# Kernel optimization log

Measured on AMD Instinct MI355X. Metric: run time of the kernel, lower is better.

The kernel has to match this reference:

```python
import jax, jax.numpy as jnp
import numpy as np

N_NODE, N_NET, E = 100000, 20000, 200000
H_NODE, H_NET, H_PIN = 64, 32, 16
O_NODE, O_NET = 32, 64


def setup_inputs() -> dict:
    key = jax.random.key(0)
    ks = jax.random.split(key, 8)
    return {
        'node_feat': jax.random.normal(ks[0], (N_NODE, H_NODE), jnp.float32),
        'net_feat': jax.random.normal(ks[1], (N_NET, H_NET), jnp.float32),
        'pin_feat': jax.random.normal(ks[2], (E, H_PIN), jnp.float32),
        'edge_node': jax.random.randint(ks[3], (E,), 0, N_NODE, jnp.int32),
        'edge_net': jax.random.randint(ks[4], (E,), 0, N_NET, jnp.int32),
        'W1': jax.random.normal(ks[5], (H_NODE, O_NET), jnp.float32) * 0.05,
        'b1': jnp.zeros((O_NET,), jnp.float32),
        'W2': jax.random.normal(ks[6], (H_PIN, H_NET * O_NODE), jnp.float32) * 0.05,
        'b2': jnp.zeros((H_NET * O_NODE,), jnp.float32),
        'b_nn': jnp.zeros((O_NODE,), jnp.float32),
    }


def reference(node_feat, net_feat, pin_feat, edge_node, edge_net, W1, b1, W2, b2, b_nn):
    ones = jnp.ones((E,), node_feat.dtype)
    # ---- relation 'pins': node -> net, DGL GraphConv with norm='both' ----
    out_deg = jnp.clip(jax.ops.segment_sum(ones, edge_node, num_segments=N_NODE), 1.0)  # src out-degree
    in_deg = jnp.clip(jax.ops.segment_sum(ones, edge_net, num_segments=N_NET), 1.0)     # dst in-degree
    src = node_feat * jax.lax.rsqrt(out_deg)[:, None]                                   # [N_node, H_node]
    agg = jax.ops.segment_sum(src[edge_node], edge_net, num_segments=N_NET)             # [N_net, H_node]
    net_out = (agg * jax.lax.rsqrt(in_deg)[:, None]) @ W1 + b1                           # [N_net, O_net]
    # ---- relation 'pinned': net -> node, DGL NNConv (mean aggregator) ----
    We = (pin_feat @ W2 + b2).reshape(E, H_NET, O_NODE)                                  # per-edge weight matrix
    msg = jnp.einsum('ei,eio->eo', net_feat[edge_net], We)                               # [E, O_node]
    node_deg = jnp.clip(jax.ops.segment_sum(ones, edge_node, num_segments=N_NODE), 1.0)
    node_out = jax.ops.segment_sum(msg, edge_node, num_segments=N_NODE) / node_deg[:, None] + b_nn
    return node_out, net_out
```

## Files before the change

kernel.cpp:

```cpp
#include <hip/hip_runtime.h>
#include <hip/hip_bf16.h>

#define N_NODE 100000
#define N_NET  20000
#define NE     200000
#define H_NODE 64
#define H_NET  32
#define H_PIN  16
#define O_NODE 32
#define O_NET  64
#define CSR_STRIDE 64


#define OFF_NETCNT  6400000
#define OFF_CSR     7680000
#define OFF_Z       17920000
#define OFF_C       38400000
#define OFF_XB      40960000
#define ZERO_BYTES  7680000

static __device__ __forceinline__ unsigned short f2bf(float f) {
    unsigned int u = __float_as_uint(f);
    u += 0x7fff + ((u >> 16) & 1);
    return (unsigned short)(u >> 16);
}
static __device__ __forceinline__ float bf2f(unsigned short h) {
    return __uint_as_float(((unsigned int)h) << 16);
}

#define EDGE_BLKS 782

__global__ void k_edge(const int* __restrict__ en, const int* __restrict__ em,
                       int* __restrict__ node_deg, int* __restrict__ net_cnt,
                       int2* __restrict__ csr) {
    int e = blockIdx.x * 256 + threadIdx.x;
    if (e < NE) {
        int v = en[e], n = em[e];
        atomicAdd(&node_deg[v << 4], 1);
        int slot = atomicAdd(&net_cnt[n << 4], 1);
        if (slot < CSR_STRIDE) csr[n * CSR_STRIDE + slot] = make_int2(e, v);
    }
}

#define DNS_Z_BLKS    1250
#define DNS_INIT_BLKS 3125
#define DNS_XB_BLKS   1563
#define ZNPB 16

__global__ void k_dense(const float* __restrict__ net_feat,
                        const float* __restrict__ node_feat,
                        const float* __restrict__ W2, const float* __restrict__ b2,
                        unsigned short* __restrict__ Zb, float* __restrict__ C,
                        unsigned short* __restrict__ Xb,
                        const float* __restrict__ b_nn,
                        float* __restrict__ out_node) {
    int t = threadIdx.x, b = blockIdx.x;
    if (b < DNS_Z_BLKS) {
        __shared__ float sy[ZNPB][H_NET];
        int base = b * ZNPB;
        for (int idx = t; idx < ZNPB * H_NET; idx += 256)
            sy[idx >> 5][idx & 31] = net_feat[(base + (idx >> 5)) * H_NET + (idx & 31)];
        __syncthreads();
        int o = t & 31, k4 = (t >> 5) & 3, rep = t >> 7;
        const float* w2p = W2 + (k4 * 4) * 1024 + o;
        float4 acc[8];
#pragma unroll
        for (int g = 0; g < 8; g++) acc[g] = make_float4(0.f, 0.f, 0.f, 0.f);
#pragma unroll 4
        for (int i = 0; i < H_NET; i++) {
            float w0 = w2p[0 * 1024 + i * 32];
            float w1 = w2p[1 * 1024 + i * 32];
            float w2v = w2p[2 * 1024 + i * 32];
            float w3 = w2p[3 * 1024 + i * 32];
#pragma unroll
            for (int g = 0; g < 8; g++) {
                float y = sy[rep * 8 + g][i];
                acc[g].x += w0 * y; acc[g].y += w1 * y;
                acc[g].z += w2v * y; acc[g].w += w3 * y;
            }
        }
#pragma unroll
        for (int g = 0; g < 8; g++) {
            int n = base + rep * 8 + g;
            ushort4 uz;
            uz.x = f2bf(acc[g].x); uz.y = f2bf(acc[g].y);
            uz.z = f2bf(acc[g].z); uz.w = f2bf(acc[g].w);
            *(ushort4*)&Zb[(size_t)n * 512 + o * 16 + k4 * 4] = uz;
        }
#pragma unroll
        for (int r = 0; r < 2; r++) {
            int idx = t + r * 256;
            int g = idx >> 5, oo = idx & 31;
            float a = 0.f;
#pragma unroll
            for (int i = 0; i < H_NET; i++) a += sy[g][i] * b2[i * 32 + oo];
            C[(base + g) * 32 + oo] = a;
        }
        return;
    }
    if (b < DNS_Z_BLKS + DNS_INIT_BLKS) {
        int idx = (b - DNS_Z_BLKS) * 256 + t;
        ((float4*)out_node)[idx] = ((const float4*)b_nn)[idx & 7];
        return;
    }
    {
        int idx = (b - DNS_Z_BLKS - DNS_INIT_BLKS) * 256 + t;
        if (idx < 400000) {
            const float4* s = (const float4*)node_feat + (size_t)idx * 4;
            float4 a0 = s[0], a1 = s[1], a2 = s[2], a3 = s[3];
            uint4 p0, p1;
            p0.x = (unsigned)f2bf(a0.x) | ((unsigned)f2bf(a0.y) << 16);
            p0.y = (unsigned)f2bf(a0.z) | ((unsigned)f2bf(a0.w) << 16);
            p0.z = (unsigned)f2bf(a1.x) | ((unsigned)f2bf(a1.y) << 16);
            p0.w = (unsigned)f2bf(a1.z) | ((unsigned)f2bf(a1.w) << 16);
            p1.x = (unsigned)f2bf(a2.x) | ((unsigned)f2bf(a2.y) << 16);
            p1.y = (unsigned)f2bf(a2.z) | ((unsigned)f2bf(a2.w) << 16);
            p1.z = (unsigned)f2bf(a3.x) | ((unsigned)f2bf(a3.y) << 16);
            p1.w = (unsigned)f2bf(a3.z) | ((unsigned)f2bf(a3.w) << 16);
            ((uint4*)Xb)[(size_t)idx * 2]     = p0;
            ((uint4*)Xb)[(size_t)idx * 2 + 1] = p1;
        }
    }
}

__global__ void k_net(const unsigned short* __restrict__ Xb,
                      const int* __restrict__ node_deg,
                      const int* __restrict__ net_cnt,
                      const int2* __restrict__ csr,
                      const float* __restrict__ W1,
                      const float* __restrict__ b1,
                      const unsigned short* __restrict__ Zb,
                      const float* __restrict__ Cg,
                      const float* __restrict__ pin_feat,
                      float* __restrict__ out_net, float* __restrict__ out_node) {
    __shared__ float  spin[4][32][16];
    __shared__ float4 srow4[4][16];
    int t = threadIdx.x;
    int w = t >> 6, l = t & 63;
    int n = blockIdx.x * 4 + w;
    int beg = n * CSR_STRIDE, deg = net_cnt[n << 4];
    int o = l & 31;
    int half = l >> 5;
    int q = l >> 4, f = l & 15;

    float z[16];
    {
        const uint4* zp = (const uint4*)&Zb[(size_t)n * 512 + o * 16];
        uint4 za = zp[0], zb = zp[1];
        unsigned int uu[8] = {za.x, za.y, za.z, za.w, zb.x, zb.y, zb.z, zb.w};
#pragma unroll
        for (int i = 0; i < 8; i++) {
            z[2 * i]     = bf2f((unsigned short)(uu[i] & 0xffffu));
            z[2 * i + 1] = bf2f((unsigned short)(uu[i] >> 16));
        }
    }
    float c = Cg[n * 32 + o];

    const uint2* xb2 = (const uint2*)Xb;
    const float4* pf4 = (const float4*)pin_feat;

    float4 acc4 = make_float4(0.f, 0.f, 0.f, 0.f);

    for (int j0 = 0; j0 < deg; j0 += 32) {
        int cnt = deg - j0; if (cnt > 32) cnt = 32;
        int vj = 0, ej = 0; float sj = 0.f;
        if (l < cnt) {
            int2 ev = csr[beg + j0 + l];
            ej = ev.x; vj = ev.y;
            float dv = (float)node_deg[vj << 4]; if (dv < 1.f) dv = 1.f;
            sj = rsqrtf(dv);
        }
        {
            int jj = l >> 2;
            int src = (jj < cnt) ? jj : cnt - 1;
            int e = __shfl(ej, src);
            float4 pv = pf4[(size_t)e * 4 + (l & 3)];
            ((float4*)&spin[w][jj][0])[l & 3] = pv;
        }
        if (cnt > 16) {
            int jj = 16 + (l >> 2);
            int src = (jj < cnt) ? jj : cnt - 1;
            int e = __shfl(ej, src);
            float4 pv = pf4[(size_t)e * 4 + (l & 3)];
            ((float4*)&spin[w][jj][0])[l & 3] = pv;
        }
        {
            int vv[4]; float ss[4];
#pragma unroll
            for (int r = 0; r < 4; r++) {
                int jj = r * 4 + q;
                int src = (jj < cnt) ? jj : cnt - 1;
                vv[r] = __shfl(vj, src);
                float sv = __shfl(sj, src);
                ss[r] = (jj < cnt) ? sv : 0.f;
            }
            uint2 xx[4];
#pragma unroll
            for (int r = 0; r < 4; r++) xx[r] = xb2[(size_t)vv[r] * 16 + f];
#pragma unroll
            for (int r = 0; r < 4; r++) {
                acc4.x += bf2f((unsigned short)(xx[r].x & 0xffffu)) * ss[r];
                acc4.y += bf2f((unsigned short)(xx[r].x >> 16)) * ss[r];
                acc4.z += bf2f((unsigned short)(xx[r].y & 0xffffu)) * ss[r];
                acc4.w += bf2f((unsigned short)(xx[r].y >> 16)) * ss[r];
            }
        }
        if (cnt > 16) {
            int vv[4]; float ss[4];
#pragma unroll
            for (int r = 0; r < 4; r++) {
                int jj = 16 + r * 4 + q;
                int src = (jj < cnt) ? jj : cnt - 1;
                vv[r] = __shfl(vj, src);
                float sv = __shfl(sj, src);
                ss[r] = (jj < cnt) ? sv : 0.f;
            }
            uint2 xx[4];
#pragma unroll
            for (int r = 0; r < 4; r++) xx[r] = xb2[(size_t)vv[r] * 16 + f];
#pragma unroll
            for (int r = 0; r < 4; r++) {
                acc4.x += bf2f((unsigned short)(xx[r].x & 0xffffu)) * ss[r];
                acc4.y += bf2f((unsigned short)(xx[r].x >> 16)) * ss[r];
                acc4.z += bf2f((unsigned short)(xx[r].y & 0xffffu)) * ss[r];
                acc4.w += bf2f((unsigned short)(xx[r].y >> 16)) * ss[r];
            }
        }
        for (int jj = 0; jj < cnt; jj += 2) {
            int je = jj + half;
            int src = (je < cnt) ? je : cnt - 1;
            int v = __shfl(vj, src);
            float sv = __shfl(sj, src);
            float inv = sv * sv;
            const float4* pr = (const float4*)&spin[w][src][0];
            float m = c;
#pragma unroll
            for (int k4 = 0; k4 < 4; k4++) {
                float4 pv = pr[k4];
                m += pv.x * z[k4 * 4 + 0] + pv.y * z[k4 * 4 + 1]
                   + pv.z * z[k4 * 4 + 2] + pv.w * z[k4 * 4 + 3];
            }
            if (je < cnt) atomicAdd(&out_node[(size_t)v * O_NODE + o], m * inv);
        }
    }
    acc4.x += __shfl_xor(acc4.x, 16); acc4.y += __shfl_xor(acc4.y, 16);
    acc4.z += __shfl_xor(acc4.z, 16); acc4.w += __shfl_xor(acc4.w, 16);
    acc4.x += __shfl_xor(acc4.x, 32); acc4.y += __shfl_xor(acc4.y, 32);
    acc4.z += __shfl_xor(acc4.z, 32); acc4.w += __shfl_xor(acc4.w, 32);
    float dn = (deg < 1) ? 1.f : (float)deg;
    float rs = rsqrtf(dn);
    if (l < 16)
        srow4[w][l] = make_float4(acc4.x * rs, acc4.y * rs, acc4.z * rs, acc4.w * rs);
    __syncthreads();
    {
        const float* a = (const float*)&srow4[w][0];
        float oacc = b1[l];
#pragma unroll 16
        for (int h = 0; h < H_NODE; h++) oacc += a[h] * W1[h * O_NET + l];
        out_net[n * O_NET + l] = oacc;
    }
}

extern "C" void kernel_launch(void* const* d_in, const int* in_sizes, int n_in,
                              void* d_out, int out_size, void* d_ws, size_t ws_size,
                              hipStream_t stream) {
    const float* node_feat = (const float*)d_in[0];
    const float* net_feat  = (const float*)d_in[1];
    const float* pin_feat  = (const float*)d_in[2];
    const int*   edge_node = (const int*)d_in[3];
    const int*   edge_net  = (const int*)d_in[4];
    const float* W1        = (const float*)d_in[5];
    const float* b1        = (const float*)d_in[6];
    const float* W2        = (const float*)d_in[7];
    const float* b2        = (const float*)d_in[8];
    const float* b_nn      = (const float*)d_in[9];

    float* out_node = (float*)d_out;
    float* out_net  = out_node + (size_t)N_NODE * O_NODE;

    char* ws = (char*)d_ws;
    int*            node_deg = (int*)ws;
    int*            net_cnt  = (int*)(ws + OFF_NETCNT);
    int2*           csr      = (int2*)(ws + OFF_CSR);
    unsigned short* Zb       = (unsigned short*)(ws + OFF_Z);
    float*          C        = (float*)(ws + OFF_C);
    unsigned short* Xb       = (unsigned short*)(ws + OFF_XB);

    (void)hipMemsetAsync(ws, 0, ZERO_BYTES, stream);

    k_edge<<<EDGE_BLKS, 256, 0, stream>>>(edge_node, edge_net,
                                          node_deg, net_cnt, csr);

    k_dense<<<DNS_Z_BLKS + DNS_INIT_BLKS + DNS_XB_BLKS, 256, 0, stream>>>(
        net_feat, node_feat, W2, b2, Zb, C, Xb, b_nn, out_node);

    k_net<<<N_NET / 4, 256, 0, stream>>>(
        Xb, node_deg, net_cnt, csr,
        W1, b1, Zb, C, pin_feat, out_net, out_node);
}
```

Before: 172.7 us.

## Build net CSR via per-block LDS histograms, scan, and deterministic scatter

```diff
diff --git a/kernel.cpp b/kernel.cpp
--- a/kernel.cpp
+++ b/kernel.cpp
@@ -11,13 +11,19 @@
 #define O_NET  64
 #define CSR_STRIDE 64
 
-
-#define OFF_NETCNT  6400000
-#define OFF_CSR     7680000
-#define OFF_Z       17920000
-#define OFF_C       38400000
-#define OFF_XB      40960000
-#define ZERO_BYTES  7680000
+#define K1_BLOCKS     64
+#define EDGES_PER_BLK 3125
+#define HIST_STRIDE   10000
+
+
+#define OFF_NETCNT  400000
+#define OFF_CSR     480000
+#define OFF_Z       10720000
+#define OFF_C       31200000
+#define OFF_XB      33760000
+#define OFF_HIST    46560000
+#define OFF_GBASE   49120000
+#define ZERO_BYTES  400000
 
 static __device__ __forceinline__ unsigned short f2bf(float f) {
     unsigned int u = __float_as_uint(f);
@@ -28,16 +34,52 @@
     return __uint_as_float(((unsigned int)h) << 16);
 }
 
-#define EDGE_BLKS 782
-
-__global__ void k_edge(const int* __restrict__ en, const int* __restrict__ em,
-                       int* __restrict__ node_deg, int* __restrict__ net_cnt,
-                       int2* __restrict__ csr) {
-    int e = blockIdx.x * 256 + threadIdx.x;
-    if (e < NE) {
-        int v = en[e], n = em[e];
-        atomicAdd(&node_deg[v << 4], 1);
-        int slot = atomicAdd(&net_cnt[n << 4], 1);
+__global__ void k_count(const int* __restrict__ en, const int* __restrict__ em,
+                        int* __restrict__ node_deg, int* __restrict__ hist) {
+    __shared__ int h[HIST_STRIDE];
+    int t = threadIdx.x, b = blockIdx.x;
+    for (int i = t; i < HIST_STRIDE; i += 256) h[i] = 0;
+    __syncthreads();
+    int e0 = b * EDGES_PER_BLK;
+    for (int k = t; k < EDGES_PER_BLK; k += 256) {
+        int e = e0 + k;
+        int n = em[e];
+        atomicAdd(&h[n >> 1], 1 << ((n & 1) * 16));
+        atomicAdd(&node_deg[en[e]], 1);
+    }
+    __syncthreads();
+    for (int i = t; i < HIST_STRIDE; i += 256) hist[b * HIST_STRIDE + i] = h[i];
+}
+
+__global__ void k_scan(const int* __restrict__ hist, int* __restrict__ gbase,
+                       int* __restrict__ net_cnt) {
+    int i = blockIdx.x * 256 + threadIdx.x;
+    if (i >= HIST_STRIDE) return;
+    int s0 = 0, s1 = 0;
+#pragma unroll 8
+    for (int b = 0; b < K1_BLOCKS; b++) {
+        int u = hist[b * HIST_STRIDE + i];
+        gbase[b * HIST_STRIDE + i] = (s0 & 0xffff) | (s1 << 16);
+        s0 += u & 0xffff; s1 += (u >> 16) & 0xffff;
+    }
+    ((int2*)net_cnt)[i] = make_int2(s0, s1);
+}
+
+__global__ void k_scatter(const int* __restrict__ en, const int* __restrict__ em,
+                          const int* __restrict__ gbase, int2* __restrict__ csr) {
+    __shared__ int h[HIST_STRIDE];
+    int t = threadIdx.x, b = blockIdx.x;
+    for (int i = t; i < HIST_STRIDE; i += 256) h[i] = 0;
+    __syncthreads();
+    int e0 = b * EDGES_PER_BLK;
+    const int* brow = gbase + b * HIST_STRIDE;
+    for (int k = t; k < EDGES_PER_BLK; k += 256) {
+        int e = e0 + k;
+        int n = em[e], v = en[e];
+        int sh = (n & 1) * 16;
+        int r    = (atomicAdd(&h[n >> 1], 1 << sh) >> sh) & 0xffff;
+        int base = (brow[n >> 1] >> sh) & 0xffff;
+        int slot = base + r;
         if (slot < CSR_STRIDE) csr[n * CSR_STRIDE + slot] = make_int2(e, v);
     }
 }
@@ -138,7 +180,7 @@
     int t = threadIdx.x;
     int w = t >> 6, l = t & 63;
     int n = blockIdx.x * 4 + w;
-    int beg = n * CSR_STRIDE, deg = net_cnt[n << 4];
+    int beg = n * CSR_STRIDE, deg = net_cnt[n];
     int o = l & 31;
     int half = l >> 5;
     int q = l >> 4, f = l & 15;
@@ -167,7 +209,7 @@
         if (l < cnt) {
             int2 ev = csr[beg + j0 + l];
             ej = ev.x; vj = ev.y;
-            float dv = (float)node_deg[vj << 4]; if (dv < 1.f) dv = 1.f;
+            float dv = (float)node_deg[vj]; if (dv < 1.f) dv = 1.f;
             sj = rsqrtf(dv);
         }
         {
@@ -285,11 +327,14 @@
     unsigned short* Zb       = (unsigned short*)(ws + OFF_Z);
     float*          C        = (float*)(ws + OFF_C);
     unsigned short* Xb       = (unsigned short*)(ws + OFF_XB);
+    int*            hist     = (int*)(ws + OFF_HIST);
+    int*            gbase    = (int*)(ws + OFF_GBASE);
 
     (void)hipMemsetAsync(ws, 0, ZERO_BYTES, stream);
 
-    k_edge<<<EDGE_BLKS, 256, 0, stream>>>(edge_node, edge_net,
-                                          node_deg, net_cnt, csr);
+    k_count<<<K1_BLOCKS, 256, 0, stream>>>(edge_node, edge_net, node_deg, hist);
+    k_scan<<<(HIST_STRIDE + 255) / 256, 256, 0, stream>>>(hist, gbase, net_cnt);
+    k_scatter<<<K1_BLOCKS, 256, 0, stream>>>(edge_node, edge_net, gbase, csr);
 
     k_dense<<<DNS_Z_BLKS + DNS_INIT_BLKS + DNS_XB_BLKS, 256, 0, stream>>>(
         net_feat, node_feat, W2, b2, Zb, C, Xb, b_nn, out_node);
```

After: 183.0 us. 1.06x slower.
